# Kernel optimization log

Measured on AMD Instinct MI355X. Metric: run time of the kernel, lower is better.

The kernel has to match this reference:

```python
import jax, jax.numpy as jnp
import numpy as np

PAD_VALUE = 0.0
DUR_MAX = 8  # exclusive upper bound on per-phoneme duration -> static padded length T*DUR_MAX


def setup_inputs() -> dict:
    key = jax.random.key(0)
    k1, k2 = jax.random.split(key)
    B, T, D = 32, 512, 384
    xs = jax.random.normal(k1, (B, T, D), dtype=jnp.float32)
    durations = jax.random.randint(k2, (B, T), 0, DUR_MAX, dtype=jnp.int32)
    return {"xs": xs, "durations": durations}


def reference(xs, durations):
    # xs: [B, T, D] phoneme embeddings; durations: [B, T] frames per phoneme.
    # Expands each phoneme embedding `duration` times along time, left-aligned,
    # padded with PAD_VALUE to a static max frame length T*DUR_MAX (jit-safe
    # upper bound on the data-dependent max length used by the torch module).
    B, T, D = xs.shape
    T_out = T * DUR_MAX

    d = durations
    # torch edge case: if ALL durations are zero, rows with zero total get 1s.
    total = d.sum()
    row_sum = d.sum(axis=1)
    d = jnp.where((total == 0) & (row_sum == 0)[:, None], 1, d)

    cum = jnp.cumsum(d, axis=1)                      # [B, T] exclusive->inclusive frame offsets
    t = jnp.arange(T_out, dtype=cum.dtype)           # [T_out]
    # frame t belongs to phoneme j where cum[j-1] <= t < cum[j]
    idx = jax.vmap(lambda c: jnp.searchsorted(c, t, side="right"))(cum)  # [B, T_out]
    valid = t[None, :] < cum[:, -1][:, None]         # [B, T_out]
    idx = jnp.minimum(idx, T - 1)                    # clamp for safe gather

    out = jnp.take_along_axis(xs, idx[:, :, None], axis=1)  # [B, T_out, D]
    return jnp.where(valid[:, :, None], out, jnp.asarray(PAD_VALUE, xs.dtype))
```

## Files before the change

kernel.cpp:

```cpp
#include <hip/hip_runtime.h>
#include <hip/hip_bf16.h>


#define B    32
#define T    512
#define D    384
#define TOUT 4096
#define CH   (D / 4)
#define F    128
#define NT   512
#define ITEMS (F * CH)

typedef float f4 __attribute__((ext_vector_type(4)));

__global__ __launch_bounds__(NT) void k_lenreg(const f4* __restrict__ xs4,
                                               const int* __restrict__ dur,
                                               f4* __restrict__ out4) {
    __shared__ int s_cum[T];
    __shared__ int s_idx[F];
    __shared__ int s_wsum[NT / 64];
    __shared__ int s_red[NT / 64];
    const int b      = blockIdx.y;
    const int frame0 = blockIdx.x * F;
    const int tid    = threadIdx.x;
    const int lane   = tid & 63;
    const int w      = tid >> 6;

    int sum = dur[b * T + tid];
    #pragma unroll
    for (int off = 1; off < 64; off <<= 1) {
        int v = __shfl_up(sum, off);
        if (lane >= off) sum += v;
    }
    if (lane == 63) s_wsum[w] = sum;
    __syncthreads();
    int prefix = 0, rowtot = 0;
    #pragma unroll
    for (int i = 0; i < NT / 64; ++i) {
        int v = s_wsum[i];
        rowtot += v;
        if (i < w) prefix += v;
    }
    int cum = sum + prefix;

    if (rowtot == 0) {
        int g = 0;
        for (int i = tid; i < B * T; i += NT) g += dur[i];
        #pragma unroll
        for (int o = 32; o > 0; o >>= 1) g += __shfl_down(g, o);
        if (lane == 0) s_red[w] = g;
        __syncthreads();
        int tot = 0;
        #pragma unroll
        for (int i = 0; i < NT / 64; ++i) tot += s_red[i];
        if (tot == 0) cum = tid + 1;
    }
    s_cum[tid] = cum;
    __syncthreads();

    const int last = s_cum[T - 1];
    int nvalid = last - frame0;
    nvalid = nvalid < 0 ? 0 : (nvalid > F ? F : nvalid);
    const int vitems = nvalid * CH;

    if (tid < nvalid) {
        int t = frame0 + tid;
        int idx = 0;
        #pragma unroll
        for (int step = T / 2; step > 0; step >>= 1)
            if (s_cum[idx + step - 1] <= t) idx += step;
        s_idx[tid] = idx < T - 1 ? idx : T - 1;
    }
    __syncthreads();

    const size_t obase = ((size_t)b * TOUT + frame0) * CH;
    const size_t ibase = (size_t)b * T * CH;

    {
        int f = tid / CH;
        int c = tid - f * CH;
        for (int item = tid; item < vitems; item += NT) {
            f4 v = xs4[ibase + (size_t)s_idx[f] * CH + c];
            __builtin_nontemporal_store(v, out4 + obase + item);
            f += NT / CH;
            c += NT - (NT / CH) * CH;
            if (c >= CH) { c -= CH; ++f; }
        }
    }
    {
        const f4 z = (f4){0.f, 0.f, 0.f, 0.f};
        for (int item = vitems + tid; item < ITEMS; item += NT)
            __builtin_nontemporal_store(z, out4 + obase + item);
    }
}

extern "C" void kernel_launch(void* const* d_in, const int* in_sizes, int n_in,
                              void* d_out, int out_size, void* d_ws, size_t ws_size,
                              hipStream_t stream) {
    const float* xs  = (const float*)d_in[0];
    const int*   dur = (const int*)d_in[1];
    float*       out = (float*)d_out;

    dim3 grid(TOUT / F, B);
    k_lenreg<<<grid, NT, 0, stream>>>((const f4*)xs, dur, (f4*)out);
}
```

Baseline: 235.0 us.

## Split into index-building kernel and unrolled streaming gather kernel

Frame-to-phoneme indices are now built once per batch row by a separate kernel that scatters phoneme ids into a shared frame map, replacing the per-block prefix scan and binary search. They are written to workspace. A second kernel with 64-frame tiles and 384 threads reads that map and does an unrolled gather/zero-store with no shared-memory setup. This removes redundant per-block scan work and syncs, at the cost of an extra launch and a round trip of the index map through global memory.

Result: no change. 237.5 us (+1.1%).

```diff
diff --git a/kernel.cpp b/kernel.cpp
--- a/kernel.cpp
+++ b/kernel.cpp
@@ -7,26 +7,20 @@
 #define D    384
 #define TOUT 4096
 #define CH   (D / 4)
-#define F    128
-#define NT   512
-#define ITEMS (F * CH)
+#define F    64
+#define NT2  384
 
 typedef float f4 __attribute__((ext_vector_type(4)));
 
-__global__ __launch_bounds__(NT) void k_lenreg(const f4* __restrict__ xs4,
-                                               const int* __restrict__ dur,
-                                               f4* __restrict__ out4) {
-    __shared__ int s_cum[T];
-    __shared__ int s_idx[F];
-    __shared__ int s_wsum[NT / 64];
-    __shared__ int s_red[NT / 64];
-    const int b      = blockIdx.y;
-    const int frame0 = blockIdx.x * F;
-    const int tid    = threadIdx.x;
-    const int lane   = tid & 63;
-    const int w      = tid >> 6;
+__global__ __launch_bounds__(T) void k_index(const int* __restrict__ dur,
+                                             int* __restrict__ idx) {
+    __shared__ int s_idx[TOUT];
+    __shared__ int s_wsum[T / 64];
+    const int b = blockIdx.x, tid = threadIdx.x;
+    const int lane = tid & 63, w = tid >> 6;
 
-    int sum = dur[b * T + tid];
+    int d = dur[b * T + tid];
+    int sum = d;
     #pragma unroll
     for (int off = 1; off < 64; off <<= 1) {
         int v = __shfl_up(sum, off);
@@ -36,7 +30,7 @@
     __syncthreads();
     int prefix = 0, rowtot = 0;
     #pragma unroll
-    for (int i = 0; i < NT / 64; ++i) {
+    for (int i = 0; i < T / 64; ++i) {
         int v = s_wsum[i];
         rowtot += v;
         if (i < w) prefix += v;
@@ -45,52 +39,44 @@
 
     if (rowtot == 0) {
         int g = 0;
-        for (int i = tid; i < B * T; i += NT) g += dur[i];
+        for (int i = tid; i < B * T; i += T) g += dur[i];
         #pragma unroll
         for (int o = 32; o > 0; o >>= 1) g += __shfl_down(g, o);
-        if (lane == 0) s_red[w] = g;
+        __syncthreads();
+        if (lane == 0) s_wsum[w] = g;
         __syncthreads();
         int tot = 0;
         #pragma unroll
-        for (int i = 0; i < NT / 64; ++i) tot += s_red[i];
-        if (tot == 0) cum = tid + 1;
+        for (int i = 0; i < T / 64; ++i) tot += s_wsum[i];
+        if (tot == 0) { d = 1; cum = tid + 1; }
     }
-    s_cum[tid] = cum;
+
+    for (int i = tid; i < TOUT; i += T) s_idx[i] = -1;
     __syncthreads();
+    for (int k = cum - d; k < cum; ++k) s_idx[k] = tid;
+    __syncthreads();
+    for (int i = tid; i < TOUT; i += T) idx[b * TOUT + i] = s_idx[i];
+}
 
-    const int last = s_cum[T - 1];
-    int nvalid = last - frame0;
-    nvalid = nvalid < 0 ? 0 : (nvalid > F ? F : nvalid);
-    const int vitems = nvalid * CH;
-
-    if (tid < nvalid) {
-        int t = frame0 + tid;
-        int idx = 0;
-        #pragma unroll
-        for (int step = T / 2; step > 0; step >>= 1)
-            if (s_cum[idx + step - 1] <= t) idx += step;
-        s_idx[tid] = idx < T - 1 ? idx : T - 1;
-    }
-    __syncthreads();
-
+__global__ __launch_bounds__(NT2) void k_stream(const f4* __restrict__ xs4,
+                                                const int* __restrict__ idx,
+                                                f4* __restrict__ out4) {
+    const int b      = blockIdx.y;
+    const int frame0 = blockIdx.x * F;
+    const int t      = threadIdx.x;
+    const int fl0    = t / CH;
+    const int c      = t - fl0 * CH;
     const size_t obase = ((size_t)b * TOUT + frame0) * CH;
     const size_t ibase = (size_t)b * T * CH;
+    const int* idxrow = idx + b * TOUT + frame0;
 
-    {
-        int f = tid / CH;
-        int c = tid - f * CH;
-        for (int item = tid; item < vitems; item += NT) {
-            f4 v = xs4[ibase + (size_t)s_idx[f] * CH + c];
-            __builtin_nontemporal_store(v, out4 + obase + item);
-            f += NT / CH;
-            c += NT - (NT / CH) * CH;
-            if (c >= CH) { c -= CH; ++f; }
-        }
-    }
-    {
-        const f4 z = (f4){0.f, 0.f, 0.f, 0.f};
-        for (int item = vitems + tid; item < ITEMS; item += NT)
-            __builtin_nontemporal_store(z, out4 + obase + item);
+    #pragma unroll
+    for (int k = 0; k < F / 4; ++k) {
+        int f = fl0 + 4 * k;
+        int j = idxrow[f];
+        f4 v = (f4){0.f, 0.f, 0.f, 0.f};
+        if (j >= 0) v = xs4[ibase + (size_t)j * CH + c];
+        __builtin_nontemporal_store(v, out4 + obase + (size_t)f * CH + c);
     }
 }
 
@@ -100,7 +86,9 @@
     const float* xs  = (const float*)d_in[0];
     const int*   dur = (const int*)d_in[1];
     float*       out = (float*)d_out;
+    int*         idx = (int*)d_ws;
 
+    k_index<<<B, T, 0, stream>>>(dur, idx);
     dim3 grid(TOUT / F, B);
-    k_lenreg<<<grid, NT, 0, stream>>>((const f4*)xs, dur, (f4*)out);
+    k_stream<<<grid, NT2, 0, stream>>>((const f4*)xs, idx, (f4*)out);
 }
```

## Replace binary search with scatter of phoneme ranges and unroll fixed-trip copy loop

Applied to the files above, without the earlier changes.

Each thread now writes its own phoneme index into the shared frame-to-phoneme map for the frames it covers inside the block's window. This replaces the shared cumsum array and per-frame binary search. Blocks lying entirely past the row's total length skip index work and only write zeros. The copy loop becomes a fixed-trip unrolled loop with a per-frame validity check and plain stores instead of nontemporal ones, trading those cache hints for more memory-level parallelism. The plain stores may change how the output write traffic behaves in cache.

Measured after the change: 227.3 us (median of 2 runs). 3.3% less time.

```diff
diff --git a/kernel.cpp b/kernel.cpp
--- a/kernel.cpp
+++ b/kernel.cpp
@@ -10,23 +10,23 @@
 #define F    128
 #define NT   512
 #define ITEMS (F * CH)
+#define ITER (ITEMS / NT)
 
 typedef float f4 __attribute__((ext_vector_type(4)));
 
 __global__ __launch_bounds__(NT) void k_lenreg(const f4* __restrict__ xs4,
                                                const int* __restrict__ dur,
                                                f4* __restrict__ out4) {
-    __shared__ int s_cum[T];
     __shared__ int s_idx[F];
     __shared__ int s_wsum[NT / 64];
-    __shared__ int s_red[NT / 64];
     const int b      = blockIdx.y;
     const int frame0 = blockIdx.x * F;
     const int tid    = threadIdx.x;
     const int lane   = tid & 63;
     const int w      = tid >> 6;
 
-    int sum = dur[b * T + tid];
+    int d = dur[b * T + tid];
+    int sum = d;
     #pragma unroll
     for (int off = 1; off < 64; off <<= 1) {
         int v = __shfl_up(sum, off);
@@ -48,49 +48,48 @@
         for (int i = tid; i < B * T; i += NT) g += dur[i];
         #pragma unroll
         for (int o = 32; o > 0; o >>= 1) g += __shfl_down(g, o);
-        if (lane == 0) s_red[w] = g;
+        __syncthreads();
+        if (lane == 0) s_wsum[w] = g;
         __syncthreads();
         int tot = 0;
         #pragma unroll
-        for (int i = 0; i < NT / 64; ++i) tot += s_red[i];
-        if (tot == 0) cum = tid + 1;
+        for (int i = 0; i < NT / 64; ++i) tot += s_wsum[i];
+        if (tot == 0) { d = 1; cum = tid + 1; rowtot = T; }
     }
-    s_cum[tid] = cum;
+
+    const size_t obase = ((size_t)b * TOUT + frame0) * CH;
+
+    if (frame0 >= rowtot) {
+        const f4 z = (f4){0.f, 0.f, 0.f, 0.f};
+        #pragma unroll
+        for (int k = 0; k < ITER; ++k)
+            out4[obase + tid + k * NT] = z;
+        return;
+    }
+
+    if (tid < F) s_idx[tid] = -1;
     __syncthreads();
-
-    const int last = s_cum[T - 1];
-    int nvalid = last - frame0;
-    nvalid = nvalid < 0 ? 0 : (nvalid > F ? F : nvalid);
-    const int vitems = nvalid * CH;
-
-    if (tid < nvalid) {
-        int t = frame0 + tid;
-        int idx = 0;
-        #pragma unroll
-        for (int step = T / 2; step > 0; step >>= 1)
-            if (s_cum[idx + step - 1] <= t) idx += step;
-        s_idx[tid] = idx < T - 1 ? idx : T - 1;
+    {
+        int a = cum - d, e = cum;
+        if (a < frame0) a = frame0;
+        int hi = frame0 + F;
+        if (e > hi) e = hi;
+        for (int k = a; k < e; ++k) s_idx[k - frame0] = tid;
     }
     __syncthreads();
 
-    const size_t obase = ((size_t)b * TOUT + frame0) * CH;
     const size_t ibase = (size_t)b * T * CH;
-
-    {
-        int f = tid / CH;
-        int c = tid - f * CH;
-        for (int item = tid; item < vitems; item += NT) {
-            f4 v = xs4[ibase + (size_t)s_idx[f] * CH + c];
-            __builtin_nontemporal_store(v, out4 + obase + item);
-            f += NT / CH;
-            c += NT - (NT / CH) * CH;
-            if (c >= CH) { c -= CH; ++f; }
-        }
-    }
-    {
-        const f4 z = (f4){0.f, 0.f, 0.f, 0.f};
-        for (int item = vitems + tid; item < ITEMS; item += NT)
-            __builtin_nontemporal_store(z, out4 + obase + item);
+    int f = tid / CH;
+    int c = tid - f * CH;
+    #pragma unroll
+    for (int k = 0; k < ITER; ++k) {
+        int j = s_idx[f];
+        f4 v = (f4){0.f, 0.f, 0.f, 0.f};
+        if (j >= 0) v = xs4[ibase + (size_t)j * CH + c];
+        out4[obase + tid + k * NT] = v;
+        f += NT / CH;
+        c += NT - (NT / CH) * CH;
+        if (c >= CH) { c -= CH; ++f; }
     }
 }
 
```
